# Kernel optimization log

Measured on AMD Instinct MI355X. Metric: run time of the kernel, lower is better.

## Reference

```python
import jax, jax.numpy as jnp
import numpy as np

B, N, D, E, H = 8, 256, 128, 32, 4
HD = D // H
EPS = 1e-5


def setup_inputs() -> dict:
    key = jax.random.key(0)
    ks = jax.random.split(key, 20)
    idx = jnp.arange(N)

    h = jax.random.normal(ks[0], (B, N, D), dtype=jnp.float32)
    adj = (jax.random.uniform(ks[1], (B, N, N)) < 0.5).astype(jnp.float32)
    adj = adj.at[:, idx, idx].set(1.0)
    edge_features = jax.random.normal(ks[2], (B, N, N, E), dtype=jnp.float32)
    src_mask = (jax.random.uniform(ks[3], (B, N, N)) < 0.7).astype(jnp.float32)
    src_mask = src_mask.at[:, idx, idx].set(1.0)

    s = 1.0 / np.sqrt(D)
    se = 1.0 / np.sqrt(E)
    p = {
        "gcn_w": jax.random.normal(ks[4], (D, D)) * s,
        "gcn_b": jnp.zeros((D,)),
        "edge_w": jax.random.normal(ks[5], (D, E)) * se,
        "edge_b": jnp.zeros((D,)),
        "wq": jax.random.normal(ks[6], (D, D)) * s,
        "wk": jax.random.normal(ks[7], (D, D)) * s,
        "wv": jax.random.normal(ks[8], (D, D)) * s,
        "bq": jnp.zeros((D,)),
        "bk": jnp.zeros((D,)),
        "bv": jnp.zeros((D,)),
        "out_w": jax.random.normal(ks[9], (D, D)) * s,
        "out_b": jnp.zeros((D,)),
        "ln_g": jnp.ones((D,)),
        "ln_b": jnp.zeros((D,)),
    }
    return {"h": h, "adj": adj, "edge_features": edge_features, "src_mask": src_mask, **p}


def reference(h, adj, edge_features, src_mask,
              gcn_w, gcn_b, edge_w, edge_b,
              wq, wk, wv, bq, bk, bv, out_w, out_b, ln_g, ln_b):
    b, n, d = h.shape

    # --- GCN branch: degree-normalized aggregation with self-loops ---
    adj_sl = adj + jnp.eye(n, dtype=h.dtype)[None]          # (B,N,N)
    deg = adj_sl.sum(-1, keepdims=True)                      # (B,N,1)
    h_agg = jnp.einsum('bnm,bmd->bnd', adj_sl, h) / deg
    h_gcn = h_agg @ gcn_w.T + gcn_b                          # (B,N,D)

    # --- edge-conditioned key/value: h_ij = h_j + edge_emb ---
    edge_emb = jnp.einsum('bnme,de->bnmd', edge_features, edge_w) + edge_b
    h_ij = h[:, None, :, :] + edge_emb                       # (B,N,N,D)

    # key padding mask: True where edge absent (masked)
    masked = (adj * src_mask) == 0                           # (B,N,N)

    # --- multi-head attention, one query per node ---
    q = (h @ wq.T + bq).reshape(b, n, H, HD)                 # (B,N,H,HD)
    k = (jnp.einsum('bnmd,ed->bnme', h_ij, wk) + bk).reshape(b, n, n, H, HD)
    v = (jnp.einsum('bnmd,ed->bnme', h_ij, wv) + bv).reshape(b, n, n, H, HD)

    scores = jnp.einsum('bnhd,bnmhd->bnhm', q, k) / np.sqrt(HD)  # (B,N,H,N)
    scores = jnp.where(masked[:, :, None, :], -jnp.inf, scores)
    attn = jax.nn.softmax(scores, axis=-1)
    o = jnp.einsum('bnhm,bnmhd->bnhd', attn, v).reshape(b, n, d)
    o = o @ out_w.T + out_b                                  # (B,N,D)

    # residual + layernorm (dropout is identity in eval)
    x = h + o
    mu = x.mean(-1, keepdims=True)
    var = ((x - mu) ** 2).mean(-1, keepdims=True)
    h_attn = ln_g * (x - mu) / jnp.sqrt(var + EPS) + ln_b

    return h_gcn + h_attn
```

## Files before the change

kernel.cpp:

```cpp
#include <hip/hip_runtime.h>
#include <hip/hip_bf16.h>

#define OFF_WQT 0
#define OFF_WKT 16384
#define OFF_WVT 32768
#define OFF_OWT 49152
#define OFF_GWT 65536
#define OFF_WKE 81920
#define OFF_WVET 86016
#define OFF_KB  90112
#define OFF_VB  90240
#define OFF_SC  90368
#define OFF_QSP 98560
#define OFF_QEP 229632
#define OFF_HG  360704
#define OFF_K0P 622848
#define OFF_V0P 753920

using half2_t = __attribute__((ext_vector_type(2))) __fp16;

static __device__ __forceinline__ half2_t u2h(unsigned int u){
  union { unsigned int u; half2_t h; } x; x.u = u; return x.h;
}
static __device__ __forceinline__ unsigned int pkf16(float a, float b){
  union { half2_t h; unsigned int u; } x;
  x.h = __builtin_amdgcn_cvt_pkrtz(a, b);
  return x.u;
}
static __device__ __forceinline__ float fdot2(unsigned int a, unsigned int b, float c){
  return __builtin_amdgcn_fdot2(u2h(a), u2h(b), c, false);
}

__global__ __launch_bounds__(256) void prep_kernel(
    const float* __restrict__ wq, const float* __restrict__ wk,
    const float* __restrict__ wv, const float* __restrict__ out_w,
    const float* __restrict__ gcn_w, const float* __restrict__ edge_w,
    const float* __restrict__ edge_b, const float* __restrict__ bk,
    const float* __restrict__ bv, float* __restrict__ ws)
{
  int blk = blockIdx.x, t = threadIdx.x;
  if (blk < 320) {
    int w = blk >> 6;
    int e0 = (blk & 63) * 256 + t;
    const float* src = (w==0) ? wq : (w==1) ? wk : (w==2) ? wv : (w==3) ? out_w : gcn_w;
    float* dst = ws + ((w==0) ? OFF_WQT : (w==1) ? OFF_WKT : (w==2) ? OFF_WVT
                      : (w==3) ? OFF_OWT : OFF_GWT);
    int k = e0 >> 7, d = e0 & 127;
    dst[e0] = src[d*128 + k];
  } else if (blk < 352) {
    int idx = blk - 320;
    int which = idx >> 4;
    int e0 = (idx & 15) * 256 + t;
    int dd = e0 >> 5, e = e0 & 31;
    const float* W = which ? wv : wk;
    float acc = 0.f;
    #pragma unroll 4
    for (int k2 = 0; k2 < 128; ++k2) acc += W[dd*128+k2] * edge_w[k2*32+e];
    if (which) ws[OFF_WVET + e*128 + dd] = acc;
    else       ws[OFF_WKE + e0] = acc;
  } else {
    int dd = t & 127;
    const float* W  = (t < 128) ? wk : wv;
    const float* bb = (t < 128) ? bk : bv;
    float acc = bb[dd];
    #pragma unroll 4
    for (int k2 = 0; k2 < 128; ++k2) acc += W[dd*128+k2] * edge_b[k2];
    ws[((t < 128) ? OFF_KB : OFF_VB) + dd] = acc;
  }
}

__global__ __launch_bounds__(256) void proj_kernel(
    const float* __restrict__ h, const float* __restrict__ adj,
    const float* __restrict__ bq, const float* __restrict__ gcn_b,
    float* __restrict__ ws)
{
  __shared__ float h_lds[256];
  __shared__ float adj_lds[512];
  __shared__ float p1[2][2][128];
  __shared__ float p2[2][2][128];
  __shared__ float p3[2][2][128];
  __shared__ float qrow[2*132];
  __shared__ float qe_l[2*132];
  __shared__ float dpart[2][2];
  __shared__ float ha_lds[2*132];

  int t = threadIdx.x;
  int d = t & 127, kh = t >> 7;
  int r0 = blockIdx.x * 2;
  int b  = r0 >> 8, n0 = r0 & 255;
  unsigned int* wsu = (unsigned int*)ws;

  if (t < 64)  ((float4*)h_lds)[t]   = ((const float4*)(h   + (size_t)r0*128))[t];
  if (t < 128) ((float4*)adj_lds)[t] = ((const float4*)(adj + (size_t)r0*256))[t];
  __syncthreads();

  {
    const float* wqT = ws + OFF_WQT;
    const float* wkT = ws + OFF_WKT;
    const float* wvT = ws + OFF_WVT;
    float aq0=0,aq1=0,ak0=0,ak1=0,av0=0,av1=0;
    #pragma unroll 4
    for (int kk = 0; kk < 64; ++kk) {
      int k = kh*64 + kk;
      float qw = wqT[k*128+d], kw = wkT[k*128+d], vw = wvT[k*128+d];
      float h0 = h_lds[k], h1 = h_lds[128+k];
      aq0 += qw*h0; aq1 += qw*h1;
      ak0 += kw*h0; ak1 += kw*h1;
      av0 += vw*h0; av1 += vw*h1;
    }
    p1[kh][0][d]=aq0; p1[kh][1][d]=aq1;
    p2[kh][0][d]=ak0; p2[kh][1][d]=ak1;
    p3[kh][0][d]=av0; p3[kh][1][d]=av1;
  }
  __syncthreads();

  {
    int i = t >> 7, dd = t & 127;
    const float inv = 0.17677669529663687f;
    qrow[i*132 + dd] = (p1[0][i][dd] + p1[1][i][dd] + bq[dd]) * inv;
  }
  {
    int i = (t >> 6) & 1, pr = t & 63;
    if (t < 128) {
      float k0 = p2[0][i][2*pr] + p2[1][i][2*pr];
      float k1 = p2[0][i][2*pr+1] + p2[1][i][2*pr+1];
      wsu[OFF_K0P + (size_t)(r0+i)*64 + pr] = pkf16(k0, k1);
    } else {
      float v0 = p3[0][i][2*pr] + p3[1][i][2*pr];
      float v1 = p3[0][i][2*pr+1] + p3[1][i][2*pr+1];
      wsu[OFF_V0P + (size_t)(r0+i)*64 + pr] = pkf16(v0, v1);
    }
  }
  __syncthreads();

  if (t < 128) {
    int i = t >> 6, pr = t & 63;
    wsu[OFF_QSP + (size_t)(r0+i)*64 + pr] = pkf16(qrow[i*132 + 2*pr], qrow[i*132 + 2*pr+1]);
  }
  {
    int i = t >> 7, he = t & 127, hh = he >> 5, e = he & 31;
    float acc = 0.f;
    #pragma unroll
    for (int j = 0; j < 32; ++j)
      acc += ws[OFF_WKE + (hh*32 + j)*32 + e] * qrow[i*132 + hh*32 + j];
    qe_l[i*132 + he] = acc;
  }
  if (t < 8) {
    int i = t >> 2, hh = t & 3;
    float acc = 0.f;
    #pragma unroll
    for (int j = 0; j < 32; ++j)
      acc += qrow[i*132 + hh*32 + j] * ws[OFF_KB + hh*32 + j];
    ws[OFF_SC + (size_t)(r0+i)*4 + hh] = acc;
  }
  {
    float ag0=0, ag1=0, dg0=0, dg1=0;
    #pragma unroll 4
    for (int mm = 0; mm < 128; ++mm) {
      int ml = kh*128 + mm;
      float hv = h[((size_t)b*256 + ml)*128 + d];
      float a0 = adj_lds[ml]       + ((ml == n0)     ? 1.0f : 0.0f);
      float a1 = adj_lds[256 + ml] + ((ml == n0 + 1) ? 1.0f : 0.0f);
      ag0 += a0*hv; ag1 += a1*hv; dg0 += a0; dg1 += a1;
    }
    p1[kh][0][d]=ag0; p1[kh][1][d]=ag1;
    if (d == 0) { dpart[kh][0]=dg0; dpart[kh][1]=dg1; }
  }
  __syncthreads();

  if (t < 128) {
    int i = t >> 6, pr = t & 63;
    wsu[OFF_QEP + (size_t)(r0+i)*64 + pr] = pkf16(qe_l[i*132 + 2*pr], qe_l[i*132 + 2*pr+1]);
  }
  {
    int i = t >> 7, dd = t & 127;
    ha_lds[i*132 + dd] = (p1[0][i][dd] + p1[1][i][dd]) / (dpart[0][i] + dpart[1][i]);
  }
  __syncthreads();

  {
    const float* gwT = ws + OFF_GWT;
    float g0=0, g1=0;
    #pragma unroll 4
    for (int kk = 0; kk < 64; ++kk) {
      int k = kh*64 + kk;
      float gw = gwT[k*128+d];
      g0 += gw * ha_lds[k];
      g1 += gw * ha_lds[132 + k];
    }
    p2[kh][0][d]=g0; p2[kh][1][d]=g1;
  }
  __syncthreads();
  {
    int i = t >> 7, dd = t & 127;
    ws[OFF_HG + (size_t)(r0+i)*128 + dd] = p2[0][i][dd] + p2[1][i][dd] + gcn_b[dd];
  }
}

__global__ __launch_bounds__(256, 4) void attn_kernel(
    const float* __restrict__ edge, const float* __restrict__ adj,
    const float* __restrict__ srcm, const float* __restrict__ h,
    const float* __restrict__ out_b, const float* __restrict__ ln_g,
    const float* __restrict__ ln_b, const float* __restrict__ ws,
    float* __restrict__ out)
{
  __shared__ unsigned int e_lds[256*18];
  __shared__ float s_lds[4*264];
  __shared__ float part4[8*132];
  __shared__ float part5[8*132];
  __shared__ float wpart[16];
  __shared__ float eb_l[132];
  __shared__ float o_l[132];
  __shared__ float px[2][128];
  __shared__ float stat[4];

  const int t  = threadIdx.x;
  const int bn = blockIdx.x;
  const int b  = bn >> 8;
  const int hh = t & 3;
  const int mq = t >> 2;
  const unsigned int* wsu = (const unsigned int*)ws;

  {
    const float4* et = (const float4*)(edge + (size_t)bn*8192);
    #pragma unroll
    for (int it = 0; it < 8; ++it) {
      int fi = it*256 + t;
      float4 v = et[fi];
      int row = fi >> 3, c4 = fi & 7;
      uint2 pk;
      pk.x = pkf16(v.x, v.y);
      pk.y = pkf16(v.z, v.w);
      *(uint2*)(e_lds + row*18 + c4*2) = pk;
    }
    float mp = adj[(size_t)bn*256 + t] * srcm[(size_t)bn*256 + t];
    e_lds[t*18 + 16] = __float_as_uint(mp);
  }
  unsigned int qs_pk[16], qe_pk[16];
  {
    const uint4* qp = (const uint4*)(wsu + OFF_QSP + (size_t)bn*64 + hh*16);
    const uint4* qe = (const uint4*)(wsu + OFF_QEP + (size_t)bn*64 + hh*16);
    #pragma unroll
    for (int j = 0; j < 4; ++j) {
      uint4 a = qp[j];
      qs_pk[4*j+0]=a.x; qs_pk[4*j+1]=a.y; qs_pk[4*j+2]=a.z; qs_pk[4*j+3]=a.w;
      uint4 c = qe[j];
      qe_pk[4*j+0]=c.x; qe_pk[4*j+1]=c.y; qe_pk[4*j+2]=c.z; qe_pk[4*j+3]=c.w;
    }
  }
  float sconst = ws[OFF_SC + (size_t)bn*4 + hh];
  __syncthreads();

  float exacc = 0.f;
  {
    const unsigned int* K0 = wsu + OFF_K0P + (size_t)b*256*64;
    for (int pass = 0; pass < 4; ++pass) {
      int mm = (pass << 6) | mq;
      float acc = sconst;
      const uint4* kr4 = (const uint4*)(K0 + (size_t)mm*64 + hh*16);
      #pragma unroll
      for (int j4 = 0; j4 < 4; ++j4) {
        uint4 kw = kr4[j4];
        acc = fdot2(qs_pk[4*j4+0], kw.x, acc);
        acc = fdot2(qs_pk[4*j4+1], kw.y, acc);
        acc = fdot2(qs_pk[4*j4+2], kw.z, acc);
        acc = fdot2(qs_pk[4*j4+3], kw.w, acc);
      }
      const uint2* er = (const uint2*)(e_lds + mm*18);
      #pragma unroll
      for (int j2 = 0; j2 < 8; ++j2) {
        uint2 w = er[j2];
        acc = fdot2(qe_pk[2*j2+0], w.x, acc);
        acc = fdot2(qe_pk[2*j2+1], w.y, acc);
      }
      float mp = __uint_as_float(e_lds[mm*18 + 16]);
      float ex = (mp == 0.0f) ? 0.0f : __expf(acc);
      s_lds[hh*264 + mm] = ex;
      exacc += ex;
    }
    exacc += __shfl_down(exacc, 4);
    exacc += __shfl_down(exacc, 8);
    exacc += __shfl_down(exacc, 16);
    exacc += __shfl_down(exacc, 32);
    if ((t & 63) < 4) wpart[(t >> 6)*4 + hh] = exacc;
  }
  __syncthreads();

  {
    int ms  = t >> 5;
    int hh4 = (t >> 3) & 3, e4 = t & 7;
    int c   = t & 31,  hh5 = c >> 3;
    float p4x=0,p4y=0,p4z=0,p4w=0;
    float p5x=0,p5y=0,p5z=0,p5w=0;
    const unsigned int* vrow = wsu + OFF_V0P + (size_t)b*256*64;
    for (int jm = 0; jm < 32; ++jm) {
      int mm = ms*32 + jm;
      float a4 = s_lds[hh4*264 + mm];
      uint2 w = *(const uint2*)(e_lds + mm*18 + e4*2);
      half2_t e0 = u2h(w.x), e1 = u2h(w.y);
      p4x += a4*(float)e0.x; p4y += a4*(float)e0.y;
      p4z += a4*(float)e1.x; p4w += a4*(float)e1.y;
      float a5 = s_lds[hh5*264 + mm];
      uint2 vv = *(const uint2*)(vrow + (size_t)mm*64 + c*2);
      half2_t v0 = u2h(vv.x), v1 = u2h(vv.y);
      p5x += a5*(float)v0.x; p5y += a5*(float)v0.y;
      p5z += a5*(float)v1.x; p5w += a5*(float)v1.y;
    }
    float4 f4; f4.x=p4x; f4.y=p4y; f4.z=p4z; f4.w=p4w;
    *(float4*)(part4 + ms*132 + hh4*32 + e4*4) = f4;
    float4 f5; f5.x=p5x; f5.y=p5y; f5.z=p5z; f5.w=p5w;
    *(float4*)(part5 + ms*132 + c*4) = f5;
  }
  __syncthreads();

  float ov_reg = 0.f;
  if (t < 128) {
    int ht = t >> 5;
    float inv = 1.0f / (wpart[ht] + wpart[4+ht] + wpart[8+ht] + wpart[12+ht]);
    float se = 0.f, s2 = 0.f;
    #pragma unroll
    for (int g = 0; g < 8; ++g) { se += part4[g*132 + t]; s2 += part5[g*132 + t]; }
    eb_l[t] = se * inv;
    ov_reg  = s2 * inv;
  }
  __syncthreads();

  if (t < 128) {
    int hd = t >> 5;
    float acc = ov_reg + ws[OFF_VB + t];
    const float* wveT = ws + OFF_WVET;
    #pragma unroll 4
    for (int e = 0; e < 32; ++e) acc += wveT[e*128 + t] * eb_l[hd*32 + e];
    o_l[t] = acc;
  }
  __syncthreads();

  {
    int d = t & 127, kh = t >> 7;
    const float* owT = ws + OFF_OWT;
    float xa = 0.f;
    #pragma unroll 4
    for (int kk = 0; kk < 64; ++kk) {
      int k = kh*64 + kk;
      xa += owT[k*128 + d] * o_l[k];
    }
    px[kh][d] = xa;
  }
  __syncthreads();

  float x = 0.f;
  if (t < 128) {
    x = px[0][t] + px[1][t] + out_b[t] + h[(size_t)bn*128 + t];
    float s = x, ss = x*x;
    #pragma unroll
    for (int off = 32; off > 0; off >>= 1) {
      s  += __shfl_down(s,  off);
      ss += __shfl_down(ss, off);
    }
    if ((t & 63) == 0) { stat[t >> 6] = s; stat[2 + (t >> 6)] = ss; }
  }
  __syncthreads();

  if (t < 128) {
    float mu   = (stat[0] + stat[1]) * (1.0f/128.0f);
    float var  = (stat[2] + stat[3]) * (1.0f/128.0f) - mu*mu;
    float rstd = rsqrtf(var + 1e-5f);
    out[(size_t)bn*128 + t] =
        ln_g[t]*(x - mu)*rstd + ln_b[t] + ws[OFF_HG + (size_t)bn*128 + t];
  }
}

extern "C" void kernel_launch(void* const* d_in, const int* in_sizes, int n_in,
                              void* d_out, int out_size, void* d_ws, size_t ws_size,
                              hipStream_t stream) {
  (void)in_sizes; (void)n_in; (void)out_size; (void)ws_size;
  const float* h     = (const float*)d_in[0];
  const float* adj   = (const float*)d_in[1];
  const float* edge  = (const float*)d_in[2];
  const float* srcm  = (const float*)d_in[3];
  const float* gcn_w = (const float*)d_in[4];
  const float* gcn_b = (const float*)d_in[5];
  const float* edge_w= (const float*)d_in[6];
  const float* edge_b= (const float*)d_in[7];
  const float* wq    = (const float*)d_in[8];
  const float* wk    = (const float*)d_in[9];
  const float* wv    = (const float*)d_in[10];
  const float* bq    = (const float*)d_in[11];
  const float* bk    = (const float*)d_in[12];
  const float* bv    = (const float*)d_in[13];
  const float* out_w = (const float*)d_in[14];
  const float* out_b = (const float*)d_in[15];
  const float* ln_g  = (const float*)d_in[16];
  const float* ln_b  = (const float*)d_in[17];

  float* ws  = (float*)d_ws;
  float* out = (float*)d_out;

  prep_kernel<<<353, 256, 0, stream>>>(wq, wk, wv, out_w, gcn_w, edge_w, edge_b, bk, bv, ws);
  proj_kernel<<<1024, 256, 0, stream>>>(h, adj, bq, gcn_b, ws);
  attn_kernel<<<2048, 256, 0, stream>>>(edge, adj, srcm, h, out_b, ln_g, ln_b, ws, out);
}
```

Baseline: 188.7 us.

## Pipeline edge-feature staging with score computation and alias LDS buffers

Splits the edge-feature load into four chunks and overlaps each chunk's global load and fp16 packing with the score computation for the previous rows, using a barrier per chunk instead of one upfront. It also aliases the small shared scratch arrays (eb_l, o_l, px, stat) onto the score buffer to cut LDS usage, and raises launch bounds to 5 blocks per CU for more occupancy. This adds extra barriers inside the score loop and risks register pressure under the tighter occupancy bound. The aliasing relies on the score buffer no longer being live when the later arrays are written.

```diff
diff --git a/kernel.cpp b/kernel.cpp
--- a/kernel.cpp
+++ b/kernel.cpp
@@ -197,7 +197,7 @@
   }
 }
 
-__global__ __launch_bounds__(256, 4) void attn_kernel(
+__global__ __launch_bounds__(256, 5) void attn_kernel(
     const float* __restrict__ edge, const float* __restrict__ adj,
     const float* __restrict__ srcm, const float* __restrict__ h,
     const float* __restrict__ out_b, const float* __restrict__ ln_g,
@@ -205,14 +205,16 @@
     float* __restrict__ out)
 {
   __shared__ unsigned int e_lds[256*18];
-  __shared__ float s_lds[4*264];
+  __shared__ float s_buf[4*264];
   __shared__ float part4[8*132];
   __shared__ float part5[8*132];
   __shared__ float wpart[16];
-  __shared__ float eb_l[132];
-  __shared__ float o_l[132];
-  __shared__ float px[2][128];
-  __shared__ float stat[4];
+
+  float* const s_lds = s_buf;
+  float* const eb_l  = s_buf;
+  float* const o_l   = s_buf + 132;
+  float* const px    = s_buf + 264;
+  float* const stat  = s_buf + 520;
 
   const int t  = threadIdx.x;
   const int bn = blockIdx.x;
@@ -221,21 +223,12 @@
   const int mq = t >> 2;
   const unsigned int* wsu = (const unsigned int*)ws;
 
-  {
-    const float4* et = (const float4*)(edge + (size_t)bn*8192);
-    #pragma unroll
-    for (int it = 0; it < 8; ++it) {
-      int fi = it*256 + t;
-      float4 v = et[fi];
-      int row = fi >> 3, c4 = fi & 7;
-      uint2 pk;
-      pk.x = pkf16(v.x, v.y);
-      pk.y = pkf16(v.z, v.w);
-      *(uint2*)(e_lds + row*18 + c4*2) = pk;
-    }
-    float mp = adj[(size_t)bn*256 + t] * srcm[(size_t)bn*256 + t];
-    e_lds[t*18 + 16] = __float_as_uint(mp);
-  }
+  const float4* et = (const float4*)(edge + (size_t)bn*8192);
+
+  float4 va = et[t];
+  float4 vb = et[256 + t];
+  float mp_my = adj[(size_t)bn*256 + t] * srcm[(size_t)bn*256 + t];
+
   unsigned int qs_pk[16], qe_pk[16];
   {
     const uint4* qp = (const uint4*)(wsu + OFF_QSP + (size_t)bn*64 + hh*16);
@@ -249,41 +242,60 @@
     }
   }
   float sconst = ws[OFF_SC + (size_t)bn*4 + hh];
-  __syncthreads();
+  const unsigned int* K0 = wsu + OFF_K0P + (size_t)b*256*64;
 
   float exacc = 0.f;
-  {
-    const unsigned int* K0 = wsu + OFF_K0P + (size_t)b*256*64;
-    for (int pass = 0; pass < 4; ++pass) {
-      int mm = (pass << 6) | mq;
-      float acc = sconst;
-      const uint4* kr4 = (const uint4*)(K0 + (size_t)mm*64 + hh*16);
-      #pragma unroll
-      for (int j4 = 0; j4 < 4; ++j4) {
-        uint4 kw = kr4[j4];
-        acc = fdot2(qs_pk[4*j4+0], kw.x, acc);
-        acc = fdot2(qs_pk[4*j4+1], kw.y, acc);
-        acc = fdot2(qs_pk[4*j4+2], kw.z, acc);
-        acc = fdot2(qs_pk[4*j4+3], kw.w, acc);
-      }
-      const uint2* er = (const uint2*)(e_lds + mm*18);
-      #pragma unroll
-      for (int j2 = 0; j2 < 8; ++j2) {
-        uint2 w = er[j2];
-        acc = fdot2(qe_pk[2*j2+0], w.x, acc);
-        acc = fdot2(qe_pk[2*j2+1], w.y, acc);
-      }
-      float mp = __uint_as_float(e_lds[mm*18 + 16]);
-      float ex = (mp == 0.0f) ? 0.0f : __expf(acc);
-      s_lds[hh*264 + mm] = ex;
-      exacc += ex;
-    }
-    exacc += __shfl_down(exacc, 4);
-    exacc += __shfl_down(exacc, 8);
-    exacc += __shfl_down(exacc, 16);
-    exacc += __shfl_down(exacc, 32);
-    if ((t & 63) < 4) wpart[(t >> 6)*4 + hh] = exacc;
-  }
+  #pragma unroll
+  for (int c = 0; c < 4; ++c) {
+    {
+      int fi = c*512 + t;
+      int row = fi >> 3, c4 = fi & 7;
+      uint2 pk;
+      pk.x = pkf16(va.x, va.y);
+      pk.y = pkf16(va.z, va.w);
+      *(uint2*)(e_lds + row*18 + c4*2) = pk;
+      int fj = fi + 256;
+      int row2 = fj >> 3, c42 = fj & 7;
+      uint2 pk2;
+      pk2.x = pkf16(vb.x, vb.y);
+      pk2.y = pkf16(vb.z, vb.w);
+      *(uint2*)(e_lds + row2*18 + c42*2) = pk2;
+    }
+    if (c == 0) e_lds[t*18 + 16] = __float_as_uint(mp_my);
+    if (c < 3) {
+      va = et[(c+1)*512 + t];
+      vb = et[(c+1)*512 + 256 + t];
+    }
+    __syncthreads();
+
+    int mm = (c << 6) | mq;
+    float acc = sconst;
+    const uint4* kr4 = (const uint4*)(K0 + (size_t)mm*64 + hh*16);
+    #pragma unroll
+    for (int j4 = 0; j4 < 4; ++j4) {
+      uint4 kw = kr4[j4];
+      acc = fdot2(qs_pk[4*j4+0], kw.x, acc);
+      acc = fdot2(qs_pk[4*j4+1], kw.y, acc);
+      acc = fdot2(qs_pk[4*j4+2], kw.z, acc);
+      acc = fdot2(qs_pk[4*j4+3], kw.w, acc);
+    }
+    const uint2* er = (const uint2*)(e_lds + mm*18);
+    #pragma unroll
+    for (int j2 = 0; j2 < 8; ++j2) {
+      uint2 w = er[j2];
+      acc = fdot2(qe_pk[2*j2+0], w.x, acc);
+      acc = fdot2(qe_pk[2*j2+1], w.y, acc);
+    }
+    float mp = __uint_as_float(e_lds[mm*18 + 16]);
+    float ex = (mp == 0.0f) ? 0.0f : __expf(acc);
+    s_lds[hh*264 + mm] = ex;
+    exacc += ex;
+  }
+  exacc += __shfl_down(exacc, 4);
+  exacc += __shfl_down(exacc, 8);
+  exacc += __shfl_down(exacc, 16);
+  exacc += __shfl_down(exacc, 32);
+  if ((t & 63) < 4) wpart[(t >> 6)*4 + hh] = exacc;
   __syncthreads();
 
   {
@@ -344,13 +356,13 @@
       int k = kh*64 + kk;
       xa += owT[k*128 + d] * o_l[k];
     }
-    px[kh][d] = xa;
+    px[kh*128 + d] = xa;
   }
   __syncthreads();
 
   float x = 0.f;
   if (t < 128) {
-    x = px[0][t] + px[1][t] + out_b[t] + h[(size_t)bn*128 + t];
+    x = px[t] + px[128 + t] + out_b[t] + h[(size_t)bn*128 + t];
     float s = x, ss = x*x;
     #pragma unroll
     for (int off = 32; off > 0; off >>= 1) {
```

Result: no change. 185.4 us (-1.7%).
